# Kernel optimization log

Measured on AMD Instinct MI355X. Metric: run time of the kernel, lower is better.

Reference implementation:

```python
import jax, jax.numpy as jnp
import numpy as np

N = 50000
E = 800000
IN_C = 128
HID = 64
HEADS = 4
OUT_C = 1
NEG_SLOPE = 0.2  # PyG GATConv default


def setup_inputs() -> dict:
    key = jax.random.key(0)
    ks = jax.random.split(key, 12)
    s = 1.0 / np.sqrt(IN_C)
    s2 = 1.0 / np.sqrt(HEADS * HID)
    return {
        "x": jax.random.normal(ks[0], (N, IN_C), jnp.float32),
        "edge_index": jax.random.randint(ks[1], (2, E), 0, N, jnp.int64),
        # layer 1 params (heads=HEADS, concat=True)
        "W1": jax.random.normal(ks[2], (IN_C, HEADS * HID), jnp.float32) * s,
        "att_src1": jax.random.normal(ks[3], (HEADS, HID), jnp.float32) * s,
        "att_dst1": jax.random.normal(ks[4], (HEADS, HID), jnp.float32) * s,
        "b1": jnp.zeros((HEADS * HID,), jnp.float32),
        # layer 2 params (heads=1, concat=False)
        "W2": jax.random.normal(ks[5], (HEADS * HID, OUT_C), jnp.float32) * s2,
        "att_src2": jax.random.normal(ks[6], (1, OUT_C), jnp.float32) * s2,
        "att_dst2": jax.random.normal(ks[7], (1, OUT_C), jnp.float32) * s2,
        "b2": jnp.zeros((OUT_C,), jnp.float32),
    }


def _gat_layer(x, src, dst, W, att_src, att_dst, b, concat):
    heads, out_c = att_src.shape
    h = (x @ W).reshape(-1, heads, out_c)          # [N, H, F]
    # per-node attention scores, gathered per edge (scalars, cheap)
    s_src = jnp.einsum('nhf,hf->nh', h, att_src)   # [N, H]
    s_dst = jnp.einsum('nhf,hf->nh', h, att_dst)
    e = jax.nn.leaky_relu(s_src[src] + s_dst[dst], NEG_SLOPE)  # [E, H]
    # segment softmax over edges sharing a destination
    m = jax.ops.segment_max(e, dst, num_segments=N)            # [N, H]
    m = jnp.where(jnp.isfinite(m), m, 0.0)
    ex = jnp.exp(e - m[dst])
    denom = jax.ops.segment_sum(ex, dst, num_segments=N)       # [N, H]
    alpha = ex / denom[dst]                                    # [E, H]
    # weighted scatter-aggregate of source features
    agg = jax.ops.segment_sum(alpha[:, :, None] * h[src], dst, num_segments=N)  # [N, H, F]
    out = agg.reshape(-1, heads * out_c) if concat else agg.mean(axis=1)
    return out + b


def reference(x, edge_index, W1, att_src1, att_dst1, b1, W2, att_src2, att_dst2, b2):
    # PyG GATConv default: add self loops
    loop = jnp.arange(N, dtype=edge_index.dtype)
    src = jnp.concatenate([edge_index[0], loop])
    dst = jnp.concatenate([edge_index[1], loop])
    h = _gat_layer(x, src, dst, W1, att_src1, att_dst1, b1, concat=True)
    h = jax.nn.elu(h)
    return _gat_layer(h, src, dst, W2, att_src2, att_dst2, b2, concat=False)
```

## Files before the change

kernel.cpp:

```cpp
#include <hip/hip_runtime.h>
#include <math.h>

#define NN 50000
#define EE 800000
#define ETOT 850000
#define NEG 0.2f
#define CAP 64
#define NBLK 782
#define NTILE 3128

typedef unsigned short ushort_t;
typedef __attribute__((ext_vector_type(8))) short bf16x8;
typedef __attribute__((ext_vector_type(4))) float f32x4;

__device__ __forceinline__ unsigned f2bf(float f) {
    unsigned u = __float_as_uint(f);
    return (u + 0x7FFFu + ((u >> 16) & 1u)) >> 16;
}
__device__ __forceinline__ unsigned cvtpk(float lo, float hi) {
    unsigned r;
    asm("v_cvt_pk_bf16_f32 %0, %1, %2" : "=v"(r) : "v"(lo), "v"(hi));
    return r;
}
__device__ __forceinline__ float blo(unsigned u) { return __uint_as_float(u << 16); }
__device__ __forceinline__ float bhi(unsigned u) { return __uint_as_float(u & 0xffff0000u); }

__device__ __forceinline__ int load_idx(const void* ei, int f64, long long pos) {
    return f64 ? (int)((const long long*)ei)[pos] : ((const int*)ei)[pos];
}

__global__ void k_fill(const void* ei, const int* __restrict__ flag,
                       int* cursor, int* __restrict__ esrc) {
    int e = blockIdx.x * blockDim.x + threadIdx.x;
    if (e >= ETOT) return;
    int f = *flag;
    int src, dst;
    if (e < EE) {
        src = load_idx(ei, f, e);
        dst = load_idx(ei, f, (long long)EE + e);
    } else {
        src = dst = e - EE;
    }
    int pos = atomicAdd(&cursor[dst], 1);
    if (pos < CAP) esrc[dst * CAP + pos] = src;
}

__global__ __launch_bounds__(256) void k_prep(const float* __restrict__ x,
                                              const float* __restrict__ W,
                                              const float* __restrict__ b1,
                                              const float* __restrict__ W2,
                                              const void* ei,
                                              bf16x8* __restrict__ Af,
                                              ushort_t* __restrict__ Wf,
                                              float* __restrict__ b1q,
                                              float* __restrict__ W2q,
                                              int* __restrict__ flag) {
    int bid = blockIdx.x, t = threadIdx.x;
    if (bid < NTILE) {
        int kt = t >> 6, lg = (t >> 4) & 3, lr = t & 15;
        int row = bid * 16 + lr;
        if (row >= NN) row = NN - 1;
        const float4* p = (const float4*)(x + (size_t)row * 128 + kt * 32 + lg * 8);
        float4 a = p[0], b = p[1];
        union { unsigned u[4]; bf16x8 v; } r;
        r.u[0] = cvtpk(a.x, a.y);
        r.u[1] = cvtpk(a.z, a.w);
        r.u[2] = cvtpk(b.x, b.y);
        r.u[3] = cvtpk(b.z, b.w);
        Af[(size_t)bid * 256 + t] = r.v;
        return;
    }
    int idx = (bid - NTILE) * 256 + t;
    if (idx < 32768) {
        int e = idx & 7, l = (idx >> 3) & 63, ct = (idx >> 9) & 15, kt = idx >> 13;
        int k = kt * 32 + (l >> 4) * 8 + e;
        int col = ct * 16 + (l & 15);
        Wf[idx] = (ushort_t)f2bf(W[k * 256 + col]);
    } else if (idx < 32768 + 64) {
        int c = idx - 32768;
        int hl = c >> 1, sub = c & 1, head = c >> 4, lrr = c & 15;
#pragma unroll
        for (int kk = 0; kk < 4; ++kk) {
            b1q[hl * 8 + sub * 4 + kk] = b1[head * 64 + lrr + 16 * kk];
            W2q[hl * 8 + sub * 4 + kk] = W2[head * 64 + lrr + 16 * kk];
        }
    } else if (idx == 32768 + 64) {
        const long long* p = (const long long*)ei;
        int ok = 1;
        for (int i = 0; i < 64; ++i) {
            long long v = p[i];
            if (v < 0 || v >= NN) ok = 0;
        }
        *flag = ok;
    }
}

__global__ __launch_bounds__(256) void k_gemm_mfma(
    const bf16x8* __restrict__ Af, const ushort_t* __restrict__ Wf,
    const float* __restrict__ aS, const float* __restrict__ aD,
    uint2* __restrict__ h1c, float* __restrict__ sS, float* __restrict__ sD) {
    int t = threadIdx.x, wid = t >> 6, l = t & 63;
    int lg = l >> 4, lr = l & 15;
    int r0 = blockIdx.x * 64;
    int tile0 = blockIdx.x * 4;
    int c0 = wid * 64;
    const bf16x8* Bv = (const bf16x8*)Wf;

    f32x4 acc[4][4] = {};
#pragma unroll
    for (int kt = 0; kt < 4; ++kt) {
        bf16x8 a[4];
#pragma unroll
        for (int rt = 0; rt < 4; ++rt)
            a[rt] = Af[(size_t)(((tile0 + rt) * 4 + kt) * 4 + lg) * 16 + lr];
#pragma unroll
        for (int ct = 0; ct < 4; ++ct) {
            bf16x8 b = Bv[(size_t)((kt * 16 + wid * 4 + ct) * 64 + l)];
#pragma unroll
            for (int rt = 0; rt < 4; ++rt)
                acc[rt][ct] = __builtin_amdgcn_mfma_f32_16x16x32_bf16(a[rt], b, acc[rt][ct], 0, 0, 0);
        }
    }
    float aSl[4], aDl[4];
#pragma unroll
    for (int ct = 0; ct < 4; ++ct) {
        aSl[ct] = aS[c0 + ct * 16 + lr];
        aDl[ct] = aD[c0 + ct * 16 + lr];
    }
#pragma unroll
    for (int rt = 0; rt < 4; ++rt) {
#pragma unroll
        for (int q = 0; q < 4; ++q) {
            int row = r0 + rt * 16 + lg * 4 + q;
            bool ok = row < NN;
            float v0 = acc[rt][0][q], v1 = acc[rt][1][q];
            float v2 = acc[rt][2][q], v3 = acc[rt][3][q];
            float p = v0 * aSl[0] + v1 * aSl[1] + v2 * aSl[2] + v3 * aSl[3];
            float dd = v0 * aDl[0] + v1 * aDl[1] + v2 * aDl[2] + v3 * aDl[3];
            uint2 u;
            u.x = cvtpk(v0, v1);
            u.y = cvtpk(v2, v3);
            if (ok) h1c[(size_t)row * 64 + wid * 16 + lr] = u;
#pragma unroll
            for (int k = 8; k >= 1; k >>= 1) {
                p += __shfl_xor(p, k, 64);
                dd += __shfl_xor(dd, k, 64);
            }
            if (ok && lr == 0) {
                sS[row * 4 + wid] = p;
                sD[row * 4 + wid] = dd;
            }
        }
    }
}

__global__ __launch_bounds__(256) void k_agg1(
    const int* __restrict__ cursor, const int* __restrict__ esrc,
    const uint4* __restrict__ h1c4, const float* __restrict__ sS,
    const float* __restrict__ sD, const float* __restrict__ b1q,
    const float* __restrict__ W2q, float* __restrict__ g) {
    __shared__ float al_lds[4][CAP][4];
    __shared__ int s_lds[4][CAP];
    int wid = threadIdx.x >> 6, lane = threadIdx.x & 63;
    int n = blockIdx.x * 4 + wid;
    if (n >= NN) return;
    int d = cursor[n];
    if (d > CAP) d = CAP;
    int dp = (d + 7) & ~7;
    float4 sd = *(const float4*)(sD + (size_t)n * 4);
    float e0 = -1e30f, e1 = -1e30f, e2 = -1e30f, e3 = -1e30f;
    int s = 0;
    if (lane < d) {
        s = esrc[n * CAP + lane];
        float4 ss = *(const float4*)(sS + (size_t)s * 4);
        e0 = ss.x + sd.x; e0 = e0 > 0.f ? e0 : NEG * e0;
        e1 = ss.y + sd.y; e1 = e1 > 0.f ? e1 : NEG * e1;
        e2 = ss.z + sd.z; e2 = e2 > 0.f ? e2 : NEG * e2;
        e3 = ss.w + sd.w; e3 = e3 > 0.f ? e3 : NEG * e3;
    }
    float m0 = e0, m1 = e1, m2 = e2, m3 = e3;
#pragma unroll
    for (int k = 32; k >= 1; k >>= 1) {
        m0 = fmaxf(m0, __shfl_xor(m0, k, 64));
        m1 = fmaxf(m1, __shfl_xor(m1, k, 64));
        m2 = fmaxf(m2, __shfl_xor(m2, k, 64));
        m3 = fmaxf(m3, __shfl_xor(m3, k, 64));
    }
    float x0 = __expf(e0 - m0);
    float x1 = __expf(e1 - m1);
    float x2 = __expf(e2 - m2);
    float x3 = __expf(e3 - m3);
    float q0 = x0, q1 = x1, q2 = x2, q3 = x3;
#pragma unroll
    for (int k = 32; k >= 1; k >>= 1) {
        q0 += __shfl_xor(q0, k, 64);
        q1 += __shfl_xor(q1, k, 64);
        q2 += __shfl_xor(q2, k, 64);
        q3 += __shfl_xor(q3, k, 64);
    }
    if (lane < dp) {
        al_lds[wid][lane][0] = x0 / q0;
        al_lds[wid][lane][1] = x1 / q1;
        al_lds[wid][lane][2] = x2 / q2;
        al_lds[wid][lane][3] = x3 / q3;
        s_lds[wid][lane] = s;
    }
    __builtin_amdgcn_s_barrier();
    int hl = lane & 31, p = lane >> 5;
    int head = hl >> 3;
    float a0 = 0.f, a1 = 0.f, a2 = 0.f, a3 = 0.f;
    float a4 = 0.f, a5 = 0.f, a6 = 0.f, a7 = 0.f;
    for (int j = 0; j < dp; j += 8) {
        int i0 = j + p, i1 = j + 2 + p, i2 = j + 4 + p, i3 = j + 6 + p;
        int s0 = s_lds[wid][i0];
        int s1 = s_lds[wid][i1];
        int s2 = s_lds[wid][i2];
        int s3 = s_lds[wid][i3];
        float w0 = al_lds[wid][i0][head];
        float w1 = al_lds[wid][i1][head];
        float w2 = al_lds[wid][i2][head];
        float w3 = al_lds[wid][i3][head];
        uint4 u0 = h1c4[(size_t)s0 * 32 + hl];
        uint4 u1 = h1c4[(size_t)s1 * 32 + hl];
        uint4 u2 = h1c4[(size_t)s2 * 32 + hl];
        uint4 u3 = h1c4[(size_t)s3 * 32 + hl];
        a0 = fmaf(w0, blo(u0.x), a0); a1 = fmaf(w0, bhi(u0.x), a1);
        a2 = fmaf(w0, blo(u0.y), a2); a3 = fmaf(w0, bhi(u0.y), a3);
        a4 = fmaf(w0, blo(u0.z), a4); a5 = fmaf(w0, bhi(u0.z), a5);
        a6 = fmaf(w0, blo(u0.w), a6); a7 = fmaf(w0, bhi(u0.w), a7);
        a0 = fmaf(w1, blo(u1.x), a0); a1 = fmaf(w1, bhi(u1.x), a1);
        a2 = fmaf(w1, blo(u1.y), a2); a3 = fmaf(w1, bhi(u1.y), a3);
        a4 = fmaf(w1, blo(u1.z), a4); a5 = fmaf(w1, bhi(u1.z), a5);
        a6 = fmaf(w1, blo(u1.w), a6); a7 = fmaf(w1, bhi(u1.w), a7);
        a0 = fmaf(w2, blo(u2.x), a0); a1 = fmaf(w2, bhi(u2.x), a1);
        a2 = fmaf(w2, blo(u2.y), a2); a3 = fmaf(w2, bhi(u2.y), a3);
        a4 = fmaf(w2, blo(u2.z), a4); a5 = fmaf(w2, bhi(u2.z), a5);
        a6 = fmaf(w2, blo(u2.w), a6); a7 = fmaf(w2, bhi(u2.w), a7);
        a0 = fmaf(w3, blo(u3.x), a0); a1 = fmaf(w3, bhi(u3.x), a1);
        a2 = fmaf(w3, blo(u3.y), a2); a3 = fmaf(w3, bhi(u3.y), a3);
        a4 = fmaf(w3, blo(u3.z), a4); a5 = fmaf(w3, bhi(u3.z), a5);
        a6 = fmaf(w3, blo(u3.w), a6); a7 = fmaf(w3, bhi(u3.w), a7);
    }
    a0 += __shfl_xor(a0, 32, 64); a1 += __shfl_xor(a1, 32, 64);
    a2 += __shfl_xor(a2, 32, 64); a3 += __shfl_xor(a3, 32, 64);
    a4 += __shfl_xor(a4, 32, 64); a5 += __shfl_xor(a5, 32, 64);
    a6 += __shfl_xor(a6, 32, 64); a7 += __shfl_xor(a7, 32, 64);
    float4 bA = ((const float4*)b1q)[hl * 2];
    float4 bB = ((const float4*)b1q)[hl * 2 + 1];
    float4 wA = ((const float4*)W2q)[hl * 2];
    float4 wB = ((const float4*)W2q)[hl * 2 + 1];
    float o0 = a0 + bA.x, o1 = a1 + bA.y, o2 = a2 + bA.z, o3 = a3 + bA.w;
    float o4 = a4 + bB.x, o5 = a5 + bB.y, o6 = a6 + bB.z, o7 = a7 + bB.w;
    o0 = o0 > 0.f ? o0 : expm1f(o0);
    o1 = o1 > 0.f ? o1 : expm1f(o1);
    o2 = o2 > 0.f ? o2 : expm1f(o2);
    o3 = o3 > 0.f ? o3 : expm1f(o3);
    o4 = o4 > 0.f ? o4 : expm1f(o4);
    o5 = o5 > 0.f ? o5 : expm1f(o5);
    o6 = o6 > 0.f ? o6 : expm1f(o6);
    o7 = o7 > 0.f ? o7 : expm1f(o7);
    float part = o0 * wA.x + o1 * wA.y + o2 * wA.z + o3 * wA.w
               + o4 * wB.x + o5 * wB.y + o6 * wB.z + o7 * wB.w;
#pragma unroll
    for (int k = 16; k >= 1; k >>= 1) part += __shfl_xor(part, k, 64);
    if (lane == 0) g[n] = part;
}

__global__ __launch_bounds__(256) void k_layer2(
    const int* __restrict__ cursor, const int* __restrict__ esrc,
    const float* __restrict__ g, const float* __restrict__ aS2,
    const float* __restrict__ aD2, const float* __restrict__ b2,
    float* __restrict__ out) {
    int wid = threadIdx.x >> 6, lane = threadIdx.x & 63;
    int n = blockIdx.x * 4 + wid;
    if (n >= NN) return;
    int d = cursor[n];
    if (d > CAP) d = CAP;
    float aS = aS2[0], aD = aD2[0];
    float dn = g[n] * aD;
    float gv = 0.f, e = -1e30f;
    if (lane < d) {
        gv = g[esrc[n * CAP + lane]];
        e = gv * aS + dn;
        e = e > 0.f ? e : NEG * e;
    }
    float m = e;
#pragma unroll
    for (int k = 32; k >= 1; k >>= 1) m = fmaxf(m, __shfl_xor(m, k, 64));
    float ex = (lane < d) ? __expf(e - m) : 0.f;
    float den = ex, ws = ex * gv;
#pragma unroll
    for (int k = 32; k >= 1; k >>= 1) {
        den += __shfl_xor(den, k, 64);
        ws += __shfl_xor(ws, k, 64);
    }
    if (lane == 0) out[n] = ws / den + b2[0];
}

extern "C" void kernel_launch(void* const* d_in, const int* in_sizes, int n_in,
                              void* d_out, int out_size, void* d_ws, size_t ws_size,
                              hipStream_t stream) {
    const float* x   = (const float*)d_in[0];
    const void*  ei  = d_in[1];
    const float* W1  = (const float*)d_in[2];
    const float* aS1 = (const float*)d_in[3];
    const float* aD1 = (const float*)d_in[4];
    const float* b1  = (const float*)d_in[5];
    const float* W2  = (const float*)d_in[6];
    const float* aS2 = (const float*)d_in[7];
    const float* aD2 = (const float*)d_in[8];
    const float* b2  = (const float*)d_in[9];
    float* out = (float*)d_out;

    char* w = (char*)d_ws;
    size_t off = 0;
    auto take = [&](size_t bytes) {
        char* p = w + off;
        off = (off + bytes + 255) & ~(size_t)255;
        return p;
    };
    int*      flag   = (int*)take(4);
    int*      cursor = (int*)take((size_t)NN * 4);
    int*      esrc   = (int*)take((size_t)NN * CAP * 4);
    float*    sS     = (float*)take((size_t)NN * 4 * 4);
    float*    sD     = (float*)take((size_t)NN * 4 * 4);
    float*    g      = (float*)take((size_t)NN * 4);
    void*     h1c    = take((size_t)NN * 64 * 8);
    bf16x8*   Af     = (bf16x8*)take((size_t)NTILE * 256 * 16);
    ushort_t* Wf     = (ushort_t*)take((size_t)128 * 256 * 2);
    float*    b1q    = (float*)take((size_t)256 * 4);
    float*    W2q    = (float*)take((size_t)256 * 4);
    (void)ws_size; (void)in_sizes; (void)n_in; (void)out_size;

    hipMemsetAsync(cursor, 0, (size_t)NN * 4, stream);
    k_prep<<<NTILE + 129, 256, 0, stream>>>(x, W1, b1, W2, ei, Af, Wf, b1q, W2q, flag);
    k_fill<<<(ETOT + 255) / 256, 256, 0, stream>>>(ei, flag, cursor, esrc);
    k_gemm_mfma<<<NBLK, 256, 0, stream>>>(Af, Wf, aS1, aD1, (uint2*)h1c, sS, sD);
    k_agg1<<<(NN + 3) / 4, 256, 0, stream>>>(cursor, esrc, (const uint4*)h1c, sS, sD, b1q, W2q, g);
    k_layer2<<<(NN + 3) / 4, 256, 0, stream>>>(cursor, esrc, g, aS2, aD2, b2, out);
}
```

Measured before the change: 169.9 us.

## Store layer-1 features head-major and map attention heads to XCDs in aggregation

The GEMM now writes h1 and the attention scores in head-major layout. k_agg1 is split so that each block handles a single head, chosen from the block index so that each pair of XCDs (L2 partitions) gathers only one head's slice of h1. The goal is better L2 locality and full 128-byte contiguous gathers per edge. The per-head partial output projections are combined through atomicAdd into a zero-initialised g, and edge source indices are stored as 16-bit values to halve index traffic. In exchange, the softmax is recomputed once per head, the kernel launches four times as many blocks, and an extra memset plus atomics are added.

```diff
diff --git a/kernel.cpp b/kernel.cpp
--- a/kernel.cpp
+++ b/kernel.cpp
@@ -30,7 +30,7 @@
 }
 
 __global__ void k_fill(const void* ei, const int* __restrict__ flag,
-                       int* cursor, int* __restrict__ esrc) {
+                       int* cursor, ushort_t* __restrict__ esrc) {
     int e = blockIdx.x * blockDim.x + threadIdx.x;
     if (e >= ETOT) return;
     int f = *flag;
@@ -42,7 +42,7 @@
         src = dst = e - EE;
     }
     int pos = atomicAdd(&cursor[dst], 1);
-    if (pos < CAP) esrc[dst * CAP + pos] = src;
+    if (pos < CAP) esrc[dst * CAP + pos] = (ushort_t)src;
 }
 
 __global__ __launch_bounds__(256) void k_prep(const float* __restrict__ x,
@@ -52,8 +52,8 @@
                                               const void* ei,
                                               bf16x8* __restrict__ Af,
                                               ushort_t* __restrict__ Wf,
-                                              float* __restrict__ b1q,
-                                              float* __restrict__ W2q,
+                                              float* __restrict__ b1s,
+                                              float* __restrict__ W2s,
                                               int* __restrict__ flag) {
     int bid = blockIdx.x, t = threadIdx.x;
     if (bid < NTILE) {
@@ -76,15 +76,13 @@
         int k = kt * 32 + (l >> 4) * 8 + e;
         int col = ct * 16 + (l & 15);
         Wf[idx] = (ushort_t)f2bf(W[k * 256 + col]);
-    } else if (idx < 32768 + 64) {
+    } else if (idx < 32768 + 256) {
         int c = idx - 32768;
-        int hl = c >> 1, sub = c & 1, head = c >> 4, lrr = c & 15;
-#pragma unroll
-        for (int kk = 0; kk < 4; ++kk) {
-            b1q[hl * 8 + sub * 4 + kk] = b1[head * 64 + lrr + 16 * kk];
-            W2q[hl * 8 + sub * 4 + kk] = W2[head * 64 + lrr + 16 * kk];
-        }
-    } else if (idx == 32768 + 64) {
+        int head = c >> 6, slot = (c >> 3) & 7, kk = c & 7;
+        int f = (kk < 4) ? (kk * 16 + 2 * slot) : ((kk - 4) * 16 + 2 * slot + 1);
+        b1s[c] = b1[head * 64 + f];
+        W2s[c] = W2[head * 64 + f];
+    } else if (idx == 32768 + 256) {
         const long long* p = (const long long*)ei;
         int ok = 1;
         for (int i = 0; i < 64; ++i) {
@@ -98,7 +96,7 @@
 __global__ __launch_bounds__(256) void k_gemm_mfma(
     const bf16x8* __restrict__ Af, const ushort_t* __restrict__ Wf,
     const float* __restrict__ aS, const float* __restrict__ aD,
-    uint2* __restrict__ h1c, float* __restrict__ sS, float* __restrict__ sD) {
+    uint2* __restrict__ h1h, float* __restrict__ sSh, float* __restrict__ sDh) {
     int t = threadIdx.x, wid = t >> 6, l = t & 63;
     int lg = l >> 4, lr = l & 15;
     int r0 = blockIdx.x * 64;
@@ -140,115 +138,85 @@
             uint2 u;
             u.x = cvtpk(v0, v1);
             u.y = cvtpk(v2, v3);
-            if (ok) h1c[(size_t)row * 64 + wid * 16 + lr] = u;
+            if (ok) h1h[((size_t)wid * NN + row) * 16 + lr] = u;
 #pragma unroll
             for (int k = 8; k >= 1; k >>= 1) {
                 p += __shfl_xor(p, k, 64);
                 dd += __shfl_xor(dd, k, 64);
             }
             if (ok && lr == 0) {
-                sS[row * 4 + wid] = p;
-                sD[row * 4 + wid] = dd;
+                sSh[wid * NN + row] = p;
+                sDh[wid * NN + row] = dd;
             }
         }
     }
 }
 
 __global__ __launch_bounds__(256) void k_agg1(
-    const int* __restrict__ cursor, const int* __restrict__ esrc,
-    const uint4* __restrict__ h1c4, const float* __restrict__ sS,
-    const float* __restrict__ sD, const float* __restrict__ b1q,
-    const float* __restrict__ W2q, float* __restrict__ g) {
-    __shared__ float al_lds[4][CAP][4];
+    const int* __restrict__ cursor, const ushort_t* __restrict__ esrc,
+    const uint4* __restrict__ h1h, const float* __restrict__ sSh,
+    const float* __restrict__ sDh, const float* __restrict__ b1s,
+    const float* __restrict__ W2s, float* __restrict__ g) {
+    __shared__ float al_lds[4][CAP];
     __shared__ int s_lds[4][CAP];
+    int b = blockIdx.x;
+    int xcd = b & 7, head = xcd >> 1, sub = xcd & 1;
+    int grp = b >> 3;
     int wid = threadIdx.x >> 6, lane = threadIdx.x & 63;
-    int n = blockIdx.x * 4 + wid;
-    if (n >= NN) return;
+    int n = grp * 8 + sub * 4 + wid;
     int d = cursor[n];
     if (d > CAP) d = CAP;
-    int dp = (d + 7) & ~7;
-    float4 sd = *(const float4*)(sD + (size_t)n * 4);
-    float e0 = -1e30f, e1 = -1e30f, e2 = -1e30f, e3 = -1e30f;
+    int dp = (d + 15) & ~15;
+    float sdn = sDh[head * NN + n];
+    float e = -1e30f;
     int s = 0;
     if (lane < d) {
         s = esrc[n * CAP + lane];
-        float4 ss = *(const float4*)(sS + (size_t)s * 4);
-        e0 = ss.x + sd.x; e0 = e0 > 0.f ? e0 : NEG * e0;
-        e1 = ss.y + sd.y; e1 = e1 > 0.f ? e1 : NEG * e1;
-        e2 = ss.z + sd.z; e2 = e2 > 0.f ? e2 : NEG * e2;
-        e3 = ss.w + sd.w; e3 = e3 > 0.f ? e3 : NEG * e3;
-    }
-    float m0 = e0, m1 = e1, m2 = e2, m3 = e3;
-#pragma unroll
-    for (int k = 32; k >= 1; k >>= 1) {
-        m0 = fmaxf(m0, __shfl_xor(m0, k, 64));
-        m1 = fmaxf(m1, __shfl_xor(m1, k, 64));
-        m2 = fmaxf(m2, __shfl_xor(m2, k, 64));
-        m3 = fmaxf(m3, __shfl_xor(m3, k, 64));
-    }
-    float x0 = __expf(e0 - m0);
-    float x1 = __expf(e1 - m1);
-    float x2 = __expf(e2 - m2);
-    float x3 = __expf(e3 - m3);
-    float q0 = x0, q1 = x1, q2 = x2, q3 = x3;
-#pragma unroll
-    for (int k = 32; k >= 1; k >>= 1) {
-        q0 += __shfl_xor(q0, k, 64);
-        q1 += __shfl_xor(q1, k, 64);
-        q2 += __shfl_xor(q2, k, 64);
-        q3 += __shfl_xor(q3, k, 64);
-    }
-    if (lane < dp) {
-        al_lds[wid][lane][0] = x0 / q0;
-        al_lds[wid][lane][1] = x1 / q1;
-        al_lds[wid][lane][2] = x2 / q2;
-        al_lds[wid][lane][3] = x3 / q3;
-        s_lds[wid][lane] = s;
-    }
-    __builtin_amdgcn_s_barrier();
-    int hl = lane & 31, p = lane >> 5;
-    int head = hl >> 3;
+        e = sSh[head * NN + s] + sdn;
+        e = e > 0.f ? e : NEG * e;
+    }
+    float m = e;
+#pragma unroll
+    for (int k = 32; k >= 1; k >>= 1) m = fmaxf(m, __shfl_xor(m, k, 64));
+    float xv = __expf(e - m);
+    float q = xv;
+#pragma unroll
+    for (int k = 32; k >= 1; k >>= 1) q += __shfl_xor(q, k, 64);
+    al_lds[wid][lane] = xv / q;
+    s_lds[wid][lane] = s;
+    int slot = lane & 7, eg = lane >> 3;
+    const uint4* hp = h1h + (size_t)head * NN * 8 + slot;
     float a0 = 0.f, a1 = 0.f, a2 = 0.f, a3 = 0.f;
     float a4 = 0.f, a5 = 0.f, a6 = 0.f, a7 = 0.f;
-    for (int j = 0; j < dp; j += 8) {
-        int i0 = j + p, i1 = j + 2 + p, i2 = j + 4 + p, i3 = j + 6 + p;
-        int s0 = s_lds[wid][i0];
-        int s1 = s_lds[wid][i1];
-        int s2 = s_lds[wid][i2];
-        int s3 = s_lds[wid][i3];
-        float w0 = al_lds[wid][i0][head];
-        float w1 = al_lds[wid][i1][head];
-        float w2 = al_lds[wid][i2][head];
-        float w3 = al_lds[wid][i3][head];
-        uint4 u0 = h1c4[(size_t)s0 * 32 + hl];
-        uint4 u1 = h1c4[(size_t)s1 * 32 + hl];
-        uint4 u2 = h1c4[(size_t)s2 * 32 + hl];
-        uint4 u3 = h1c4[(size_t)s3 * 32 + hl];
-        a0 = fmaf(w0, blo(u0.x), a0); a1 = fmaf(w0, bhi(u0.x), a1);
-        a2 = fmaf(w0, blo(u0.y), a2); a3 = fmaf(w0, bhi(u0.y), a3);
-        a4 = fmaf(w0, blo(u0.z), a4); a5 = fmaf(w0, bhi(u0.z), a5);
-        a6 = fmaf(w0, blo(u0.w), a6); a7 = fmaf(w0, bhi(u0.w), a7);
-        a0 = fmaf(w1, blo(u1.x), a0); a1 = fmaf(w1, bhi(u1.x), a1);
-        a2 = fmaf(w1, blo(u1.y), a2); a3 = fmaf(w1, bhi(u1.y), a3);
-        a4 = fmaf(w1, blo(u1.z), a4); a5 = fmaf(w1, bhi(u1.z), a5);
-        a6 = fmaf(w1, blo(u1.w), a6); a7 = fmaf(w1, bhi(u1.w), a7);
-        a0 = fmaf(w2, blo(u2.x), a0); a1 = fmaf(w2, bhi(u2.x), a1);
-        a2 = fmaf(w2, blo(u2.y), a2); a3 = fmaf(w2, bhi(u2.y), a3);
-        a4 = fmaf(w2, blo(u2.z), a4); a5 = fmaf(w2, bhi(u2.z), a5);
-        a6 = fmaf(w2, blo(u2.w), a6); a7 = fmaf(w2, bhi(u2.w), a7);
-        a0 = fmaf(w3, blo(u3.x), a0); a1 = fmaf(w3, bhi(u3.x), a1);
-        a2 = fmaf(w3, blo(u3.y), a2); a3 = fmaf(w3, bhi(u3.y), a3);
-        a4 = fmaf(w3, blo(u3.z), a4); a5 = fmaf(w3, bhi(u3.z), a5);
-        a6 = fmaf(w3, blo(u3.w), a6); a7 = fmaf(w3, bhi(u3.w), a7);
-    }
-    a0 += __shfl_xor(a0, 32, 64); a1 += __shfl_xor(a1, 32, 64);
-    a2 += __shfl_xor(a2, 32, 64); a3 += __shfl_xor(a3, 32, 64);
-    a4 += __shfl_xor(a4, 32, 64); a5 += __shfl_xor(a5, 32, 64);
-    a6 += __shfl_xor(a6, 32, 64); a7 += __shfl_xor(a7, 32, 64);
-    float4 bA = ((const float4*)b1q)[hl * 2];
-    float4 bB = ((const float4*)b1q)[hl * 2 + 1];
-    float4 wA = ((const float4*)W2q)[hl * 2];
-    float4 wB = ((const float4*)W2q)[hl * 2 + 1];
+    for (int j = 0; j < dp; j += 16) {
+        int iA = j + eg, iB = j + 8 + eg;
+        float wA = al_lds[wid][iA];
+        float wB = al_lds[wid][iB];
+        int sA = s_lds[wid][iA];
+        int sB = s_lds[wid][iB];
+        uint4 uA = hp[(size_t)sA * 8];
+        uint4 uB = hp[(size_t)sB * 8];
+        a0 = fmaf(wA, blo(uA.x), a0); a1 = fmaf(wA, bhi(uA.x), a1);
+        a2 = fmaf(wA, blo(uA.y), a2); a3 = fmaf(wA, bhi(uA.y), a3);
+        a4 = fmaf(wA, blo(uA.z), a4); a5 = fmaf(wA, bhi(uA.z), a5);
+        a6 = fmaf(wA, blo(uA.w), a6); a7 = fmaf(wA, bhi(uA.w), a7);
+        a0 = fmaf(wB, blo(uB.x), a0); a1 = fmaf(wB, bhi(uB.x), a1);
+        a2 = fmaf(wB, blo(uB.y), a2); a3 = fmaf(wB, bhi(uB.y), a3);
+        a4 = fmaf(wB, blo(uB.z), a4); a5 = fmaf(wB, bhi(uB.z), a5);
+        a6 = fmaf(wB, blo(uB.w), a6); a7 = fmaf(wB, bhi(uB.w), a7);
+    }
+    a0 += __shfl_xor(a0, 8, 64);  a0 += __shfl_xor(a0, 16, 64); a0 += __shfl_xor(a0, 32, 64);
+    a1 += __shfl_xor(a1, 8, 64);  a1 += __shfl_xor(a1, 16, 64); a1 += __shfl_xor(a1, 32, 64);
+    a2 += __shfl_xor(a2, 8, 64);  a2 += __shfl_xor(a2, 16, 64); a2 += __shfl_xor(a2, 32, 64);
+    a3 += __shfl_xor(a3, 8, 64);  a3 += __shfl_xor(a3, 16, 64); a3 += __shfl_xor(a3, 32, 64);
+    a4 += __shfl_xor(a4, 8, 64);  a4 += __shfl_xor(a4, 16, 64); a4 += __shfl_xor(a4, 32, 64);
+    a5 += __shfl_xor(a5, 8, 64);  a5 += __shfl_xor(a5, 16, 64); a5 += __shfl_xor(a5, 32, 64);
+    a6 += __shfl_xor(a6, 8, 64);  a6 += __shfl_xor(a6, 16, 64); a6 += __shfl_xor(a6, 32, 64);
+    a7 += __shfl_xor(a7, 8, 64);  a7 += __shfl_xor(a7, 16, 64); a7 += __shfl_xor(a7, 32, 64);
+    const float4* bp = (const float4*)(b1s + head * 64 + slot * 8);
+    const float4* wp = (const float4*)(W2s + head * 64 + slot * 8);
+    float4 bA = bp[0], bB = bp[1];
+    float4 wA4 = wp[0], wB4 = wp[1];
     float o0 = a0 + bA.x, o1 = a1 + bA.y, o2 = a2 + bA.z, o3 = a3 + bA.w;
     float o4 = a4 + bB.x, o5 = a5 + bB.y, o6 = a6 + bB.z, o7 = a7 + bB.w;
     o0 = o0 > 0.f ? o0 : expm1f(o0);
@@ -259,15 +227,16 @@
     o5 = o5 > 0.f ? o5 : expm1f(o5);
     o6 = o6 > 0.f ? o6 : expm1f(o6);
     o7 = o7 > 0.f ? o7 : expm1f(o7);
-    float part = o0 * wA.x + o1 * wA.y + o2 * wA.z + o3 * wA.w
-               + o4 * wB.x + o5 * wB.y + o6 * wB.z + o7 * wB.w;
-#pragma unroll
-    for (int k = 16; k >= 1; k >>= 1) part += __shfl_xor(part, k, 64);
-    if (lane == 0) g[n] = part;
+    float part = o0 * wA4.x + o1 * wA4.y + o2 * wA4.z + o3 * wA4.w
+               + o4 * wB4.x + o5 * wB4.y + o6 * wB4.z + o7 * wB4.w;
+    part += __shfl_xor(part, 1, 64);
+    part += __shfl_xor(part, 2, 64);
+    part += __shfl_xor(part, 4, 64);
+    if (lane == 0) atomicAdd(&g[n], part);
 }
 
 __global__ __launch_bounds__(256) void k_layer2(
-    const int* __restrict__ cursor, const int* __restrict__ esrc,
+    const int* __restrict__ cursor, const ushort_t* __restrict__ esrc,
     const float* __restrict__ g, const float* __restrict__ aS2,
     const float* __restrict__ aD2, const float* __restrict__ b2,
     float* __restrict__ out) {
@@ -321,21 +290,22 @@
     };
     int*      flag   = (int*)take(4);
     int*      cursor = (int*)take((size_t)NN * 4);
-    int*      esrc   = (int*)take((size_t)NN * CAP * 4);
-    float*    sS     = (float*)take((size_t)NN * 4 * 4);
-    float*    sD     = (float*)take((size_t)NN * 4 * 4);
+    ushort_t* esrc   = (ushort_t*)take((size_t)NN * CAP * 2);
+    float*    sSh    = (float*)take((size_t)4 * NN * 4);
+    float*    sDh    = (float*)take((size_t)4 * NN * 4);
     float*    g      = (float*)take((size_t)NN * 4);
-    void*     h1c    = take((size_t)NN * 64 * 8);
+    void*     h1h    = take((size_t)4 * NN * 128);
     bf16x8*   Af     = (bf16x8*)take((size_t)NTILE * 256 * 16);
     ushort_t* Wf     = (ushort_t*)take((size_t)128 * 256 * 2);
-    float*    b1q    = (float*)take((size_t)256 * 4);
-    float*    W2q    = (float*)take((size_t)256 * 4);
+    float*    b1s    = (float*)take((size_t)256 * 4);
+    float*    W2s    = (float*)take((size_t)256 * 4);
     (void)ws_size; (void)in_sizes; (void)n_in; (void)out_size;
 
     hipMemsetAsync(cursor, 0, (size_t)NN * 4, stream);
-    k_prep<<<NTILE + 129, 256, 0, stream>>>(x, W1, b1, W2, ei, Af, Wf, b1q, W2q, flag);
+    hipMemsetAsync(g, 0, (size_t)NN * 4, stream);
+    k_prep<<<NTILE + 130, 256, 0, stream>>>(x, W1, b1, W2, ei, Af, Wf, b1s, W2s, flag);
     k_fill<<<(ETOT + 255) / 256, 256, 0, stream>>>(ei, flag, cursor, esrc);
-    k_gemm_mfma<<<NBLK, 256, 0, stream>>>(Af, Wf, aS1, aD1, (uint2*)h1c, sS, sD);
-    k_agg1<<<(NN + 3) / 4, 256, 0, stream>>>(cursor, esrc, (const uint4*)h1c, sS, sD, b1q, W2q, g);
+    k_gemm_mfma<<<NBLK, 256, 0, stream>>>(Af, Wf, aS1, aD1, (uint2*)h1h, sSh, sDh);
+    k_agg1<<<(NN / 4) * 4, 256, 0, stream>>>(cursor, esrc, (const uint4*)h1h, sSh, sDh, b1s, W2s, g);
     k_layer2<<<(NN + 3) / 4, 256, 0, stream>>>(cursor, esrc, g, aS2, aD2, b2, out);
 }
```

Result: slower. 220.0 us (+29.5%).
